# Performance work log

Measured on AMD Instinct MI355X. Metric: run time of the kernel, lower is better.

## Reference

```python
import jax, jax.numpy as jnp
import numpy as np

EPS = 1e-5

def _mvn(feat):
    # instance-norm style mean/std over spatial dims; torch .var is unbiased (ddof=1)
    b, c = feat.shape[:2]
    flat = feat.reshape(b, c, -1)
    mu = flat.mean(-1)[:, :, None, None]
    std = jnp.sqrt(flat.var(-1, ddof=1) + EPS)[:, :, None, None]
    return (feat - mu) / std

def setup_inputs() -> dict:
    key = jax.random.key(0)
    ks = jax.random.split(key, 10)
    B, C, H, W = 4, 512, 64, 64
    sc = 0.05
    return {
        "content": jax.random.normal(ks[0], (B, C, H, W), jnp.float32),
        "style": jax.random.normal(ks[1], (B, C, H, W), jnp.float32),
        "content_key": jax.random.normal(ks[2], (B, C, H, W), jnp.float32),
        "style_key": jax.random.normal(ks[3], (B, C, H, W), jnp.float32),
        "Wf": jax.random.normal(ks[4], (C, C), jnp.float32) * sc,
        "bf": jax.random.normal(ks[5], (C,), jnp.float32) * sc,
        "Wg": jax.random.normal(ks[6], (C, C), jnp.float32) * sc,
        "bg": jax.random.normal(ks[7], (C,), jnp.float32) * sc,
        "Wh": jax.random.normal(ks[8], (C, C), jnp.float32) * sc,
        "bh": jax.random.normal(ks[9], (C,), jnp.float32) * sc,
    }

def reference(content, style, content_key, style_key, Wf, bf, Wg, bg, Wh, bh):
    b, C, h, w = content.shape
    hs, ws = style.shape[2], style.shape[3]
    n, m = h * w, hs * ws
    # 1x1 convs are per-pixel linear maps
    Fq = jnp.einsum('oc,bcn->bno', Wf, content_key.reshape(b, -1, n)) + bf      # [b, n, ck]
    G = jnp.einsum('oc,bcn->bon', Wg, style_key.reshape(b, -1, m)) + bg[:, None]  # [b, ck, m]
    V = jnp.einsum('oc,bcn->bno', Wh, style.reshape(b, C, m)) + bh              # [b, m, C]
    S = jax.nn.softmax(jnp.einsum('bnc,bcm->bnm', Fq, G), axis=-1)              # [b, n, m]
    mean = jnp.einsum('bnm,bmc->bnc', S, V)                                     # attention-weighted mean
    m2 = jnp.einsum('bnm,bmc->bnc', S, V * V)                                   # weighted second moment
    std = jnp.sqrt(jax.nn.relu(m2 - mean * mean))
    mean = mean.reshape(b, h, w, C).transpose(0, 3, 1, 2)
    std = std.reshape(b, h, w, C).transpose(0, 3, 1, 2)
    return std * _mvn(content) + mean
```

## Files before the change

### kernel.cpp

```cpp
#include <hip/hip_runtime.h>
#include <math.h>

#define BATCH 4
#define C 512
#define N 4096
#define M 4096

typedef __attribute__((ext_vector_type(8))) short short8;
typedef __attribute__((ext_vector_type(8))) __bf16 bf16x8;
typedef __attribute__((ext_vector_type(4))) float f32x4;

static __device__ __forceinline__ unsigned short f2bf(float x) {
    unsigned u = __float_as_uint(x);
    u += 0x7fff + ((u >> 16) & 1);
    return (unsigned short)(u >> 16);
}
static __device__ __forceinline__ float bf2f(unsigned short h) {
    return __uint_as_float(((unsigned)h) << 16);
}
static __device__ __forceinline__ f32x4 mfma_bf16(short8 a, short8 b, f32x4 c) {
    return __builtin_amdgcn_mfma_f32_16x16x32_bf16(
        __builtin_bit_cast(bf16x8, a), __builtin_bit_cast(bf16x8, b), c, 0, 0, 0);
}

__global__ __launch_bounds__(256) void wsplit_kernel(
    const float* __restrict__ W, unsigned short* __restrict__ hi,
    unsigned short* __restrict__ lo)
{
    int i = blockIdx.x * 256 + threadIdx.x;
    float v = W[i];
    unsigned short h = f2bf(v);
    hi[i] = h;
    lo[i] = f2bf(v - bf2f(h));
}

__global__ __launch_bounds__(256) void linear_fg_mfma(
    const float* __restrict__ in,
    const unsigned short* __restrict__ Whi, const unsigned short* __restrict__ Wlo,
    const float* __restrict__ bias,
    unsigned short* __restrict__ out_hi, unsigned short* __restrict__ out_lo)
{
    __shared__ float in_s[32][68];
    __shared__ __align__(16) unsigned short wh_s[64][40];
    __shared__ __align__(16) unsigned short wl_s[64][40];
    const int tid = threadIdx.x;
    const int n0 = blockIdx.x * 64, o0 = blockIdx.y * 64;
    const int w = tid >> 6, lane = tid & 63;
    const int wrow = w >> 1, wcol = w & 1;
    const int lr = lane & 15, q = lane >> 4;
    f32x4 acc[2][2];
    #pragma unroll
    for (int i = 0; i < 2; ++i)
        #pragma unroll
        for (int j = 0; j < 2; ++j) acc[i][j] = (f32x4){0.f, 0.f, 0.f, 0.f};

    for (int kc = 0; kc < C; kc += 32) {
        __syncthreads();
        #pragma unroll
        for (int it = 0; it < 2; ++it) {
            int idx = tid + it * 256;
            int k = idx >> 4, seg = idx & 15;
            *(float4*)&in_s[k][seg * 4] =
                *(const float4*)&in[(size_t)(kc + k) * N + n0 + seg * 4];
        }
        {
            int o = tid >> 2, sg = tid & 3;
            *(float4*)&wh_s[o][sg * 8] = *(const float4*)&Whi[(size_t)(o0 + o) * 512 + kc + sg * 8];
            *(float4*)&wl_s[o][sg * 8] = *(const float4*)&Wlo[(size_t)(o0 + o) * 512 + kc + sg * 8];
        }
        __syncthreads();
        short8 ah[2], al[2], bh[2], bl[2];
        #pragma unroll
        for (int i = 0; i < 2; ++i) {
            int n = wrow * 32 + i * 16 + lr;
            #pragma unroll
            for (int j = 0; j < 8; ++j) {
                float f = in_s[q * 8 + j][n];
                unsigned short h = f2bf(f);
                ah[i][j] = (short)h;
                al[i][j] = (short)f2bf(f - bf2f(h));
            }
        }
        #pragma unroll
        for (int j = 0; j < 2; ++j) {
            int o = wcol * 32 + j * 16 + lr;
            bh[j] = *(const short8*)&wh_s[o][q * 8];
            bl[j] = *(const short8*)&wl_s[o][q * 8];
        }
        #pragma unroll
        for (int i = 0; i < 2; ++i)
            #pragma unroll
            for (int j = 0; j < 2; ++j) {
                acc[i][j] = mfma_bf16(ah[i], bh[j], acc[i][j]);
                acc[i][j] = mfma_bf16(ah[i], bl[j], acc[i][j]);
                acc[i][j] = mfma_bf16(al[i], bh[j], acc[i][j]);
            }
    }
    #pragma unroll
    for (int i = 0; i < 2; ++i)
        #pragma unroll
        for (int j = 0; j < 2; ++j) {
            int o = o0 + wcol * 32 + j * 16 + lr;
            float bo = bias[o];
            #pragma unroll
            for (int r = 0; r < 4; ++r) {
                int n = n0 + wrow * 32 + i * 16 + q * 4 + r;
                float v = acc[i][j][r] + bo;
                unsigned short h = f2bf(v);
                out_hi[(size_t)n * 512 + o] = h;
                out_lo[(size_t)n * 512 + o] = f2bf(v - bf2f(h));
            }
        }
}

__global__ __launch_bounds__(256) void linear_v_mfma(
    const float* __restrict__ in,
    const unsigned short* __restrict__ Whi, const unsigned short* __restrict__ Wlo,
    const float* __restrict__ bias,
    unsigned short* __restrict__ vhT, unsigned short* __restrict__ v2hT,
    unsigned short* __restrict__ v2lT)
{
    __shared__ float in_s[32][68];
    __shared__ __align__(16) unsigned short wh_s[64][40];
    __shared__ __align__(16) unsigned short wl_s[64][40];
    const int tid = threadIdx.x;
    const int m0 = blockIdx.x * 64, o0 = blockIdx.y * 64;
    const int w = tid >> 6, lane = tid & 63;
    const int wrow = w >> 1, wcol = w & 1;
    const int lr = lane & 15, q = lane >> 4;
    f32x4 acc[2][2];
    #pragma unroll
    for (int i = 0; i < 2; ++i)
        #pragma unroll
        for (int j = 0; j < 2; ++j) acc[i][j] = (f32x4){0.f, 0.f, 0.f, 0.f};

    for (int kc = 0; kc < C; kc += 32) {
        __syncthreads();
        #pragma unroll
        for (int it = 0; it < 2; ++it) {
            int idx = tid + it * 256;
            int k = idx >> 4, seg = idx & 15;
            *(float4*)&in_s[k][seg * 4] =
                *(const float4*)&in[(size_t)(kc + k) * N + m0 + seg * 4];
        }
        {
            int o = tid >> 2, sg = tid & 3;
            *(float4*)&wh_s[o][sg * 8] = *(const float4*)&Whi[(size_t)(o0 + o) * 512 + kc + sg * 8];
            *(float4*)&wl_s[o][sg * 8] = *(const float4*)&Wlo[(size_t)(o0 + o) * 512 + kc + sg * 8];
        }
        __syncthreads();
        short8 ah[2], al[2], bh[2], bl[2];
        #pragma unroll
        for (int i = 0; i < 2; ++i) {
            int o = wrow * 32 + i * 16 + lr;
            ah[i] = *(const short8*)&wh_s[o][q * 8];
            al[i] = *(const short8*)&wl_s[o][q * 8];
        }
        #pragma unroll
        for (int j = 0; j < 2; ++j) {
            int m = wcol * 32 + j * 16 + lr;
            #pragma unroll
            for (int t = 0; t < 8; ++t) {
                float f = in_s[q * 8 + t][m];
                unsigned short h = f2bf(f);
                bh[j][t] = (short)h;
                bl[j][t] = (short)f2bf(f - bf2f(h));
            }
        }
        #pragma unroll
        for (int i = 0; i < 2; ++i)
            #pragma unroll
            for (int j = 0; j < 2; ++j) {
                acc[i][j] = mfma_bf16(ah[i], bh[j], acc[i][j]);
                acc[i][j] = mfma_bf16(ah[i], bl[j], acc[i][j]);
                acc[i][j] = mfma_bf16(al[i], bh[j], acc[i][j]);
            }
    }
    #pragma unroll
    for (int i = 0; i < 2; ++i)
        #pragma unroll
        for (int r = 0; r < 4; ++r) {
            int o = o0 + wrow * 32 + i * 16 + q * 4 + r;
            float bo = bias[o];
            #pragma unroll
            for (int j = 0; j < 2; ++j) {
                int m = m0 + wcol * 32 + j * 16 + lr;
                float v = acc[i][j][r] + bo;
                unsigned short vh = f2bf(v);
                float vhf = bf2f(vh);
                float vsq = vhf * vhf;
                unsigned short v2h = f2bf(vsq);
                unsigned short v2l = f2bf(vsq - bf2f(v2h));
                size_t off = (size_t)o * M + m;
                vhT[off] = vh;
                v2hT[off] = v2h;
                v2lT[off] = v2l;
            }
        }
}

__global__ __launch_bounds__(256) void logits_mfma_kernel(
    const unsigned short* __restrict__ Ah, const unsigned short* __restrict__ Al,
    const unsigned short* __restrict__ Bh, const unsigned short* __restrict__ Bl,
    float* __restrict__ S)
{
    __shared__ __align__(16) unsigned short Ah_s[128 * 40];
    __shared__ __align__(16) unsigned short Al_s[128 * 40];
    __shared__ __align__(16) unsigned short Bh_s[128 * 40];
    __shared__ __align__(16) unsigned short Bl_s[128 * 40];
    const int tid = threadIdx.x;
    const int n0 = blockIdx.y * 128, m0 = blockIdx.x * 128;
    const int w = tid >> 6, lane = tid & 63;
    const int wrow = w >> 1, wcol = w & 1;
    const int lr = lane & 15, q = lane >> 4;
    f32x4 acc[4][4];
    #pragma unroll
    for (int i = 0; i < 4; ++i)
        #pragma unroll
        for (int j = 0; j < 4; ++j)
            acc[i][j] = (f32x4){0.f, 0.f, 0.f, 0.f};

    for (int kc = 0; kc < C; kc += 32) {
        __syncthreads();
        #pragma unroll
        for (int it = 0; it < 2; ++it) {
            int idx = tid + it * 256;
            int row = idx >> 2, seg = idx & 3;
            int ldso = row * 40 + seg * 8;
            int go = kc + seg * 8;
            *(float4*)&Ah_s[ldso] = *(const float4*)&Ah[(size_t)(n0 + row) * C + go];
            *(float4*)&Al_s[ldso] = *(const float4*)&Al[(size_t)(n0 + row) * C + go];
            *(float4*)&Bh_s[ldso] = *(const float4*)&Bh[(size_t)(m0 + row) * C + go];
            *(float4*)&Bl_s[ldso] = *(const float4*)&Bl[(size_t)(m0 + row) * C + go];
        }
        __syncthreads();
        short8 ah[4], al[4], bh[4], bl[4];
        #pragma unroll
        for (int i = 0; i < 4; ++i) {
            int ro = (wrow * 64 + i * 16 + lr) * 40 + q * 8;
            int co = (wcol * 64 + i * 16 + lr) * 40 + q * 8;
            ah[i] = *(const short8*)&Ah_s[ro];
            al[i] = *(const short8*)&Al_s[ro];
            bh[i] = *(const short8*)&Bh_s[co];
            bl[i] = *(const short8*)&Bl_s[co];
        }
        #pragma unroll
        for (int i = 0; i < 4; ++i)
            #pragma unroll
            for (int j = 0; j < 4; ++j) {
                acc[i][j] = mfma_bf16(ah[i], bh[j], acc[i][j]);
                acc[i][j] = mfma_bf16(ah[i], bl[j], acc[i][j]);
                acc[i][j] = mfma_bf16(al[i], bh[j], acc[i][j]);
            }
    }
    #pragma unroll
    for (int i = 0; i < 4; ++i) {
        int nb = n0 + wrow * 64 + i * 16 + q * 4;
        #pragma unroll
        for (int j = 0; j < 4; ++j) {
            int m = m0 + wcol * 64 + j * 16 + lr;
            #pragma unroll
            for (int r = 0; r < 4; ++r)
                S[(size_t)(nb + r) * M + m] = acc[i][j][r];
        }
    }
}

__global__ __launch_bounds__(256) void rowstat_p_kernel(
    const float* __restrict__ S, unsigned short* __restrict__ P,
    float* __restrict__ rsum)
{
    const int n = blockIdx.x;
    const int tid = threadIdx.x;
    const float* row = S + (size_t)n * M;
    float v[16];
    #pragma unroll
    for (int i = 0; i < 16; ++i) v[i] = row[tid + i * 256];
    float lm = -INFINITY;
    #pragma unroll
    for (int i = 0; i < 16; ++i) lm = fmaxf(lm, v[i]);
    #pragma unroll
    for (int off = 32; off > 0; off >>= 1) lm = fmaxf(lm, __shfl_xor(lm, off, 64));
    __shared__ float red[4];
    __shared__ float redsum[4];
    const int wid = tid >> 6, lane = tid & 63;
    if (lane == 0) red[wid] = lm;
    __syncthreads();
    const float rm = fmaxf(fmaxf(red[0], red[1]), fmaxf(red[2], red[3]));
    float ls = 0.f;
    unsigned short* prow = P + (size_t)n * M;
    #pragma unroll
    for (int i = 0; i < 16; ++i) {
        float p = __expf(v[i] - rm);
        unsigned short pb = f2bf(p);
        prow[tid + i * 256] = pb;
        ls += bf2f(pb);
    }
    #pragma unroll
    for (int off = 32; off > 0; off >>= 1) ls += __shfl_xor(ls, off, 64);
    if (lane == 0) redsum[wid] = ls;
    __syncthreads();
    if (tid == 0) rsum[n] = redsum[0] + redsum[1] + redsum[2] + redsum[3];
}

__global__ __launch_bounds__(256) void apply_mfma_kernel(
    const unsigned short* __restrict__ P, const unsigned short* __restrict__ VhT,
    const unsigned short* __restrict__ V2hT, const unsigned short* __restrict__ V2lT,
    const float* __restrict__ rsum,
    float* __restrict__ meanw, float* __restrict__ stdw)
{
    const int b = blockIdx.z;
    P    += (size_t)b * N * M;
    VhT  += (size_t)b * C * M;
    V2hT += (size_t)b * C * M;
    V2lT += (size_t)b * C * M;
    rsum += (size_t)b * N;
    meanw += (size_t)b * N * C;
    stdw  += (size_t)b * N * C;

    __shared__ __align__(16) unsigned short P_s[128 * 40];
    __shared__ __align__(16) unsigned short Vh_s[64 * 40];
    __shared__ __align__(16) unsigned short V2h_s[64 * 40];
    __shared__ __align__(16) unsigned short V2l_s[64 * 40];
    const int tid = threadIdx.x;
    const int c0 = blockIdx.x * 64, n0 = blockIdx.y * 128;
    const int w = tid >> 6, lane = tid & 63;
    const int wrow = w >> 1, wcol = w & 1;
    const int lr = lane & 15, q = lane >> 4;
    f32x4 accm[4][2], acc2[4][2];
    #pragma unroll
    for (int i = 0; i < 4; ++i)
        #pragma unroll
        for (int j = 0; j < 2; ++j) {
            accm[i][j] = (f32x4){0.f, 0.f, 0.f, 0.f};
            acc2[i][j] = (f32x4){0.f, 0.f, 0.f, 0.f};
        }

    for (int mc = 0; mc < M; mc += 32) {
        __syncthreads();
        #pragma unroll
        for (int it = 0; it < 2; ++it) {
            int idx = tid + it * 256;
            int row = idx >> 2, seg = idx & 3;
            *(float4*)&P_s[row * 40 + seg * 8] =
                *(const float4*)&P[(size_t)(n0 + row) * M + mc + seg * 8];
        }
        {
            int row = tid >> 2, seg = tid & 3;
            int ldso = row * 40 + seg * 8;
            size_t go = (size_t)(c0 + row) * M + mc + seg * 8;
            *(float4*)&Vh_s[ldso]  = *(const float4*)&VhT[go];
            *(float4*)&V2h_s[ldso] = *(const float4*)&V2hT[go];
            *(float4*)&V2l_s[ldso] = *(const float4*)&V2lT[go];
        }
        __syncthreads();
        short8 a[4], bmat[2], b2h[2], b2l[2];
        #pragma unroll
        for (int i = 0; i < 4; ++i)
            a[i] = *(const short8*)&P_s[(wrow * 64 + i * 16 + lr) * 40 + q * 8];
        #pragma unroll
        for (int j = 0; j < 2; ++j) {
            int co = (wcol * 32 + j * 16 + lr) * 40 + q * 8;
            bmat[j] = *(const short8*)&Vh_s[co];
            b2h[j]  = *(const short8*)&V2h_s[co];
            b2l[j]  = *(const short8*)&V2l_s[co];
        }
        #pragma unroll
        for (int i = 0; i < 4; ++i)
            #pragma unroll
            for (int j = 0; j < 2; ++j) {
                accm[i][j] = mfma_bf16(a[i], bmat[j], accm[i][j]);
                acc2[i][j] = mfma_bf16(a[i], b2h[j],  acc2[i][j]);
                acc2[i][j] = mfma_bf16(a[i], b2l[j],  acc2[i][j]);
            }
    }
    #pragma unroll
    for (int i = 0; i < 4; ++i) {
        int nb = n0 + wrow * 64 + i * 16 + q * 4;
        #pragma unroll
        for (int j = 0; j < 2; ++j) {
            int c = c0 + wcol * 32 + j * 16 + lr;
            #pragma unroll
            for (int r = 0; r < 4; ++r) {
                int n = nb + r;
                float inv = 1.0f / rsum[n];
                float mn = accm[i][j][r] * inv;
                float m2 = acc2[i][j][r] * inv;
                float sd = sqrtf(fmaxf(m2 - mn * mn, 0.f));
                meanw[(size_t)n * C + c] = mn;
                stdw[(size_t)n * C + c]  = sd;
            }
        }
    }
}

__global__ __launch_bounds__(256) void mvn_kernel(
    const float* __restrict__ content, float* __restrict__ mu, float* __restrict__ rstd)
{
    const int b = blockIdx.y;
    content += (size_t)b * C * N;
    mu   += (size_t)b * C;
    rstd += (size_t)b * C;
    const int c = blockIdx.x;
    const int tid = threadIdx.x;
    const float* row = content + (size_t)c * N;
    float s = 0.f, ss = 0.f;
    for (int i = tid; i < N; i += 256) {
        float v = row[i];
        s += v;
        ss = fmaf(v, v, ss);
    }
    #pragma unroll
    for (int off = 32; off > 0; off >>= 1) {
        s  += __shfl_xor(s,  off, 64);
        ss += __shfl_xor(ss, off, 64);
    }
    __shared__ float rs[4], rss[4];
    const int wid = tid >> 6, lane = tid & 63;
    if (lane == 0) { rs[wid] = s; rss[wid] = ss; }
    __syncthreads();
    if (tid == 0) {
        float st = rs[0] + rs[1] + rs[2] + rs[3];
        float sst = rss[0] + rss[1] + rss[2] + rss[3];
        float m = st / (float)N;
        float var = (sst - st * st / (float)N) / (float)(N - 1);
        mu[c] = m;
        rstd[c] = rsqrtf(var + 1e-5f);
    }
}

__global__ __launch_bounds__(256) void final_kernel(
    const float* __restrict__ content, const float* __restrict__ meanw,
    const float* __restrict__ stdw, const float* __restrict__ mu,
    const float* __restrict__ rstd, float* __restrict__ out)
{
    const int b = blockIdx.z;
    content += (size_t)b * C * N;
    out     += (size_t)b * C * N;
    meanw   += (size_t)b * N * C;
    stdw    += (size_t)b * N * C;
    mu   += (size_t)b * C;
    rstd += (size_t)b * C;

    __shared__ float mn_s[32][33], sd_s[32][33];
    const int tid = threadIdx.x;
    const int n0 = blockIdx.x * 32;
    const int c0 = blockIdx.y * 32;
    const int tx = tid & 31, ty = tid >> 5;
    #pragma unroll
    for (int i = 0; i < 4; ++i) {
        int n = ty + i * 8;
        mn_s[tx][n] = meanw[(size_t)(n0 + n) * C + c0 + tx];
        sd_s[tx][n] = stdw [(size_t)(n0 + n) * C + c0 + tx];
    }
    __syncthreads();
    #pragma unroll
    for (int i = 0; i < 4; ++i) {
        int c = ty + i * 8;
        float m = mu[c0 + c], r = rstd[c0 + c];
        size_t off = (size_t)(c0 + c) * N + n0 + tx;
        float x = content[off];
        out[off] = sd_s[c][tx] * (x - m) * r + mn_s[c][tx];
    }
}

extern "C" void kernel_launch(void* const* d_in, const int* in_sizes, int n_in,
                              void* d_out, int out_size, void* d_ws, size_t ws_size,
                              hipStream_t stream)
{
    const float* content = (const float*)d_in[0];
    const float* style   = (const float*)d_in[1];
    const float* ckey    = (const float*)d_in[2];
    const float* skey    = (const float*)d_in[3];
    const float* Wf      = (const float*)d_in[4];
    const float* bf      = (const float*)d_in[5];
    const float* Wg      = (const float*)d_in[6];
    const float* bg      = (const float*)d_in[7];
    const float* Wh      = (const float*)d_in[8];
    const float* bh      = (const float*)d_in[9];
    float* out = (float*)d_out;

    const size_t sz_w  = (size_t)512 * 512 * 2;
    const size_t sz_S  = (size_t)N * M * 4;
    const size_t sz_FG = (size_t)N * C * 2;
    const size_t sz_P1 = (size_t)N * M * 2;
    const size_t sz_V1 = (size_t)C * M * 2;
    const size_t sz_r1 = (size_t)N * 4;
    const size_t sz_m1 = (size_t)N * C * 4;
    const size_t sz_u1 = (size_t)C * 4;
    auto need = [&](size_t nb) {
        return 6 * sz_w + sz_S + 4 * sz_FG +
               nb * (sz_P1 + 3 * sz_V1 + sz_r1 + 2 * sz_m1 + 2 * sz_u1) + (size_t)64 * 1024;
    };
    const bool batched = ws_size >= need(BATCH);
    const size_t NB = batched ? BATCH : 1;

    char* p = (char*)d_ws;
    auto alloc = [&](size_t bytes) {
        char* r = p;
        p += (bytes + 255) & ~(size_t)255;
        return r;
    };
    unsigned short* WfH = (unsigned short*)alloc(sz_w);
    unsigned short* WfL = (unsigned short*)alloc(sz_w);
    unsigned short* WgH = (unsigned short*)alloc(sz_w);
    unsigned short* WgL = (unsigned short*)alloc(sz_w);
    unsigned short* WhH = (unsigned short*)alloc(sz_w);
    unsigned short* WhL = (unsigned short*)alloc(sz_w);
    float* S = (float*)alloc(sz_S);
    unsigned short* Fh = (unsigned short*)alloc(sz_FG);
    unsigned short* Fl = (unsigned short*)alloc(sz_FG);
    unsigned short* Gh = (unsigned short*)alloc(sz_FG);
    unsigned short* Gl = (unsigned short*)alloc(sz_FG);
    unsigned short* P    = (unsigned short*)alloc(NB * sz_P1);
    unsigned short* VhT  = (unsigned short*)alloc(NB * sz_V1);
    unsigned short* V2hT = (unsigned short*)alloc(NB * sz_V1);
    unsigned short* V2lT = (unsigned short*)alloc(NB * sz_V1);
    float* rsum  = (float*)alloc(NB * sz_r1);
    float* meanw = (float*)alloc(NB * sz_m1);
    float* stdw  = (float*)alloc(NB * sz_m1);
    float* mu    = (float*)alloc(NB * sz_u1);
    float* rstd  = (float*)alloc(NB * sz_u1);

    wsplit_kernel<<<dim3(1024), 256, 0, stream>>>(Wf, WfH, WfL);
    wsplit_kernel<<<dim3(1024), 256, 0, stream>>>(Wg, WgH, WgL);
    wsplit_kernel<<<dim3(1024), 256, 0, stream>>>(Wh, WhH, WhL);

    for (int b = 0; b < BATCH; ++b) {
        const size_t fo = (size_t)b * C * N;
        const size_t bi = batched ? (size_t)b : 0;
        linear_fg_mfma<<<dim3(N / 64, C / 64), 256, 0, stream>>>(ckey + fo, WfH, WfL, bf, Fh, Fl);
        linear_fg_mfma<<<dim3(M / 64, C / 64), 256, 0, stream>>>(skey + fo, WgH, WgL, bg, Gh, Gl);
        linear_v_mfma<<<dim3(M / 64, C / 64), 256, 0, stream>>>(style + fo, WhH, WhL, bh,
                                                                VhT + bi * C * M,
                                                                V2hT + bi * C * M,
                                                                V2lT + bi * C * M);
        logits_mfma_kernel<<<dim3(M / 128, N / 128), 256, 0, stream>>>(Fh, Fl, Gh, Gl, S);
        rowstat_p_kernel<<<dim3(N), 256, 0, stream>>>(S, P + bi * (size_t)N * M, rsum + bi * N);
        if (!batched) {
            apply_mfma_kernel<<<dim3(C / 64, N / 128, 1), 256, 0, stream>>>(
                P, VhT, V2hT, V2lT, rsum, meanw, stdw);
            mvn_kernel<<<dim3(C, 1), 256, 0, stream>>>(content + fo, mu, rstd);
            final_kernel<<<dim3(N / 32, C / 32, 1), 256, 0, stream>>>(
                content + fo, meanw, stdw, mu, rstd, out + fo);
        }
    }
    if (batched) {
        apply_mfma_kernel<<<dim3(C / 64, N / 128, BATCH), 256, 0, stream>>>(
            P, VhT, V2hT, V2lT, rsum, meanw, stdw);
        mvn_kernel<<<dim3(C, BATCH), 256, 0, stream>>>(content, mu, rstd);
        final_kernel<<<dim3(N / 32, C / 32, BATCH), 256, 0, stream>>>(
            content, meanw, stdw, mu, rstd, out);
    }
}
```

Before: 1.197 ms.

## Split attention-apply reduction over M per batch and add a combine kernel

Removes the workspace-size-dependent batched path and runs the whole pipeline per batch. The P·V apply kernel now splits the M reduction into four slices, each writing unnormalized partial sums into the reused logits buffer S. A new combine kernel sums the slices, normalizes by the row sum and computes mean and std. This raises per-batch block count and lowers workspace use, at the cost of extra partial-sum writes and reads plus an additional launch per batch.

```diff
diff --git a/kernel.cpp b/kernel.cpp
--- a/kernel.cpp
+++ b/kernel.cpp
@@ -5,6 +5,7 @@
 #define C 512
 #define N 4096
 #define M 4096
+#define MSPLIT 4
 
 typedef __attribute__((ext_vector_type(8))) short short8;
 typedef __attribute__((ext_vector_type(8))) __bf16 bf16x8;
@@ -303,27 +304,18 @@
     if (tid == 0) rsum[n] = redsum[0] + redsum[1] + redsum[2] + redsum[3];
 }
 
-__global__ __launch_bounds__(256) void apply_mfma_kernel(
+__global__ __launch_bounds__(256) void apply_partial_kernel(
     const unsigned short* __restrict__ P, const unsigned short* __restrict__ VhT,
     const unsigned short* __restrict__ V2hT, const unsigned short* __restrict__ V2lT,
-    const float* __restrict__ rsum,
-    float* __restrict__ meanw, float* __restrict__ stdw)
-{
-    const int b = blockIdx.z;
-    P    += (size_t)b * N * M;
-    VhT  += (size_t)b * C * M;
-    V2hT += (size_t)b * C * M;
-    V2lT += (size_t)b * C * M;
-    rsum += (size_t)b * N;
-    meanw += (size_t)b * N * C;
-    stdw  += (size_t)b * N * C;
-
+    float* __restrict__ accm_p, float* __restrict__ acc2_p)
+{
     __shared__ __align__(16) unsigned short P_s[128 * 40];
     __shared__ __align__(16) unsigned short Vh_s[64 * 40];
     __shared__ __align__(16) unsigned short V2h_s[64 * 40];
     __shared__ __align__(16) unsigned short V2l_s[64 * 40];
     const int tid = threadIdx.x;
     const int c0 = blockIdx.x * 64, n0 = blockIdx.y * 128;
+    const int z = blockIdx.z;
     const int w = tid >> 6, lane = tid & 63;
     const int wrow = w >> 1, wcol = w & 1;
     const int lr = lane & 15, q = lane >> 4;
@@ -336,7 +328,8 @@
             acc2[i][j] = (f32x4){0.f, 0.f, 0.f, 0.f};
         }
 
-    for (int mc = 0; mc < M; mc += 32) {
+    const int mbeg = z * (M / MSPLIT);
+    for (int mc = mbeg; mc < mbeg + M / MSPLIT; mc += 32) {
         __syncthreads();
         #pragma unroll
         for (int it = 0; it < 2; ++it) {
@@ -374,6 +367,7 @@
                 acc2[i][j] = mfma_bf16(a[i], b2l[j],  acc2[i][j]);
             }
     }
+    const size_t pbase = (size_t)z * N * C;
     #pragma unroll
     for (int i = 0; i < 4; ++i) {
         int nb = n0 + wrow * 64 + i * 16 + q * 4;
@@ -382,25 +376,47 @@
             int c = c0 + wcol * 32 + j * 16 + lr;
             #pragma unroll
             for (int r = 0; r < 4; ++r) {
-                int n = nb + r;
-                float inv = 1.0f / rsum[n];
-                float mn = accm[i][j][r] * inv;
-                float m2 = acc2[i][j][r] * inv;
-                float sd = sqrtf(fmaxf(m2 - mn * mn, 0.f));
-                meanw[(size_t)n * C + c] = mn;
-                stdw[(size_t)n * C + c]  = sd;
-            }
-        }
-    }
+                size_t off = pbase + (size_t)(nb + r) * C + c;
+                accm_p[off] = accm[i][j][r];
+                acc2_p[off] = acc2[i][j][r];
+            }
+        }
+    }
+}
+
+__global__ __launch_bounds__(256) void combine_kernel(
+    const float* __restrict__ accm_p, const float* __restrict__ acc2_p,
+    const float* __restrict__ rsum, float* __restrict__ meanw,
+    float* __restrict__ stdw)
+{
+    const size_t idx = ((size_t)blockIdx.x * 256 + threadIdx.x) * 4;
+    const int n = (int)(idx >> 9);
+    const float inv = 1.0f / rsum[n];
+    float sm[4] = {0.f, 0.f, 0.f, 0.f}, s2[4] = {0.f, 0.f, 0.f, 0.f};
+    #pragma unroll
+    for (int z = 0; z < MSPLIT; ++z) {
+        float4 a = *(const float4*)&accm_p[(size_t)z * N * C + idx];
+        float4 b = *(const float4*)&acc2_p[(size_t)z * N * C + idx];
+        sm[0] += a.x; sm[1] += a.y; sm[2] += a.z; sm[3] += a.w;
+        s2[0] += b.x; s2[1] += b.y; s2[2] += b.z; s2[3] += b.w;
+    }
+    float4 mnv, sdv;
+    float* mp = (float*)&mnv;
+    float* sp = (float*)&sdv;
+    #pragma unroll
+    for (int k = 0; k < 4; ++k) {
+        float mn = sm[k] * inv;
+        float m2 = s2[k] * inv;
+        mp[k] = mn;
+        sp[k] = sqrtf(fmaxf(m2 - mn * mn, 0.f));
+    }
+    *(float4*)&meanw[idx] = mnv;
+    *(float4*)&stdw[idx]  = sdv;
 }
 
 __global__ __launch_bounds__(256) void mvn_kernel(
     const float* __restrict__ content, float* __restrict__ mu, float* __restrict__ rstd)
 {
-    const int b = blockIdx.y;
-    content += (size_t)b * C * N;
-    mu   += (size_t)b * C;
-    rstd += (size_t)b * C;
     const int c = blockIdx.x;
     const int tid = threadIdx.x;
     const float* row = content + (size_t)c * N;
@@ -434,14 +450,6 @@
     const float* __restrict__ stdw, const float* __restrict__ mu,
     const float* __restrict__ rstd, float* __restrict__ out)
 {
-    const int b = blockIdx.z;
-    content += (size_t)b * C * N;
-    out     += (size_t)b * C * N;
-    meanw   += (size_t)b * N * C;
-    stdw    += (size_t)b * N * C;
-    mu   += (size_t)b * C;
-    rstd += (size_t)b * C;
-
     __shared__ float mn_s[32][33], sd_s[32][33];
     const int tid = threadIdx.x;
     const int n0 = blockIdx.x * 32;
@@ -483,17 +491,8 @@
     const size_t sz_w  = (size_t)512 * 512 * 2;
     const size_t sz_S  = (size_t)N * M * 4;
     const size_t sz_FG = (size_t)N * C * 2;
-    const size_t sz_P1 = (size_t)N * M * 2;
-    const size_t sz_V1 = (size_t)C * M * 2;
-    const size_t sz_r1 = (size_t)N * 4;
-    const size_t sz_m1 = (size_t)N * C * 4;
-    const size_t sz_u1 = (size_t)C * 4;
-    auto need = [&](size_t nb) {
-        return 6 * sz_w + sz_S + 4 * sz_FG +
-               nb * (sz_P1 + 3 * sz_V1 + sz_r1 + 2 * sz_m1 + 2 * sz_u1) + (size_t)64 * 1024;
-    };
-    const bool batched = ws_size >= need(BATCH);
-    const size_t NB = batched ? BATCH : 1;
+    const size_t sz_P  = (size_t)N * M * 2;
+    const size_t sz_V  = (size_t)C * M * 2;
 
     char* p = (char*)d_ws;
     auto alloc = [&](size_t bytes) {
@@ -512,15 +511,18 @@
     unsigned short* Fl = (unsigned short*)alloc(sz_FG);
     unsigned short* Gh = (unsigned short*)alloc(sz_FG);
     unsigned short* Gl = (unsigned short*)alloc(sz_FG);
-    unsigned short* P    = (unsigned short*)alloc(NB * sz_P1);
-    unsigned short* VhT  = (unsigned short*)alloc(NB * sz_V1);
-    unsigned short* V2hT = (unsigned short*)alloc(NB * sz_V1);
-    unsigned short* V2lT = (unsigned short*)alloc(NB * sz_V1);
-    float* rsum  = (float*)alloc(NB * sz_r1);
-    float* meanw = (float*)alloc(NB * sz_m1);
-    float* stdw  = (float*)alloc(NB * sz_m1);
-    float* mu    = (float*)alloc(NB * sz_u1);
-    float* rstd  = (float*)alloc(NB * sz_u1);
+    unsigned short* P    = (unsigned short*)alloc(sz_P);
+    unsigned short* VhT  = (unsigned short*)alloc(sz_V);
+    unsigned short* V2hT = (unsigned short*)alloc(sz_V);
+    unsigned short* V2lT = (unsigned short*)alloc(sz_V);
+    float* rsum  = (float*)alloc((size_t)N * 4);
+    float* meanw = (float*)alloc((size_t)N * C * 4);
+    float* stdw  = (float*)alloc((size_t)N * C * 4);
+    float* mu    = (float*)alloc((size_t)C * 4);
+    float* rstd  = (float*)alloc((size_t)C * 4);
+
+    float* accm_p = S;
+    float* acc2_p = S + (size_t)MSPLIT * N * C;
 
     wsplit_kernel<<<dim3(1024), 256, 0, stream>>>(Wf, WfH, WfL);
     wsplit_kernel<<<dim3(1024), 256, 0, stream>>>(Wg, WgH, WgL);
@@ -528,28 +530,18 @@
 
     for (int b = 0; b < BATCH; ++b) {
         const size_t fo = (size_t)b * C * N;
-        const size_t bi = batched ? (size_t)b : 0;
         linear_fg_mfma<<<dim3(N / 64, C / 64), 256, 0, stream>>>(ckey + fo, WfH, WfL, bf, Fh, Fl);
         linear_fg_mfma<<<dim3(M / 64, C / 64), 256, 0, stream>>>(skey + fo, WgH, WgL, bg, Gh, Gl);
         linear_v_mfma<<<dim3(M / 64, C / 64), 256, 0, stream>>>(style + fo, WhH, WhL, bh,
-                                                                VhT + bi * C * M,
-                                                                V2hT + bi * C * M,
-                                                                V2lT + bi * C * M);
+                                                                VhT, V2hT, V2lT);
         logits_mfma_kernel<<<dim3(M / 128, N / 128), 256, 0, stream>>>(Fh, Fl, Gh, Gl, S);
-        rowstat_p_kernel<<<dim3(N), 256, 0, stream>>>(S, P + bi * (size_t)N * M, rsum + bi * N);
-        if (!batched) {
-            apply_mfma_kernel<<<dim3(C / 64, N / 128, 1), 256, 0, stream>>>(
-                P, VhT, V2hT, V2lT, rsum, meanw, stdw);
-            mvn_kernel<<<dim3(C, 1), 256, 0, stream>>>(content + fo, mu, rstd);
-            final_kernel<<<dim3(N / 32, C / 32, 1), 256, 0, stream>>>(
-                content + fo, meanw, stdw, mu, rstd, out + fo);
-        }
-    }
-    if (batched) {
-        apply_mfma_kernel<<<dim3(C / 64, N / 128, BATCH), 256, 0, stream>>>(
-            P, VhT, V2hT, V2lT, rsum, meanw, stdw);
-        mvn_kernel<<<dim3(C, BATCH), 256, 0, stream>>>(content, mu, rstd);
-        final_kernel<<<dim3(N / 32, C / 32, BATCH), 256, 0, stream>>>(
-            content, meanw, stdw, mu, rstd, out);
-    }
-}
+        rowstat_p_kernel<<<dim3(N), 256, 0, stream>>>(S, P, rsum);
+        apply_partial_kernel<<<dim3(C / 64, N / 128, MSPLIT), 256, 0, stream>>>(
+            P, VhT, V2hT, V2lT, accm_p, acc2_p);
+        combine_kernel<<<dim3(N * C / 1024), 256, 0, stream>>>(
+            accm_p, acc2_p, rsum, meanw, stdw);
+        mvn_kernel<<<dim3(C), 256, 0, stream>>>(content + fo, mu, rstd);
+        final_kernel<<<dim3(N / 32, C / 32), 256, 0, stream>>>(
+            content + fo, meanw, stdw, mu, rstd, out + fo);
+    }
+}
```

Result: faster. 1.148 ms (-4.1%).
